# Kernel optimization log

Hardware: AMD Instinct MI355X
Metric: run time of the kernel (lower is better)

The kernel has to match this reference:

```python
import jax, jax.numpy as jnp
import numpy as np


def setup_inputs() -> dict:
    key = jax.random.key(0)
    ks = jax.random.split(key, 8)
    B, L, E = 4096, 200, 64
    H1, H2 = 80, 40
    q = jax.random.normal(ks[0], (B, 1, E), dtype=jnp.float32)
    k = jax.random.normal(ks[1], (B, L, E), dtype=jnp.float32)
    v = jax.random.normal(ks[2], (B, L, E), dtype=jnp.float32)
    mask = jax.random.randint(ks[3], (B, L, 1), 0, 2).astype(bool)
    # Linear weights stored as [in, out] (torch stores [out, in]; math identical)
    W1 = jax.random.normal(ks[4], (4 * E, H1), dtype=jnp.float32) * 0.05
    b1 = jnp.zeros((H1,), dtype=jnp.float32)
    W2 = jax.random.normal(ks[5], (H1, H2), dtype=jnp.float32) * 0.05
    b2 = jnp.zeros((H2,), dtype=jnp.float32)
    Wf = jax.random.normal(ks[6], (H2, 1), dtype=jnp.float32) * 0.05
    bf = jnp.zeros((1,), dtype=jnp.float32)
    return {"q": q, "k": k, "v": v, "mask": mask,
            "W1": W1, "b1": b1, "W2": W2, "b2": b2, "Wf": Wf, "bf": bf}


def reference(q, k, v, mask, W1, b1, W2, b2, Wf, bf):
    # q: [B,1,E] broadcast to [B,L,E]
    qr = jnp.broadcast_to(q, k.shape)
    info = jnp.concatenate([qr, k, qr - k, qr * k], axis=-1)  # [B,L,4E]
    info = info @ W1 + b1                                      # [B,L,H1]
    info = info @ W2 + b2                                      # [B,L,H2]
    info = jax.nn.sigmoid(info)  # single sigmoid after the dense stack, as in source
    logits = info @ Wf + bf                                    # [B,L,1]
    logits = jnp.where(mask, -jnp.inf, logits)
    score = jax.nn.softmax(logits, axis=1)                     # softmax over history dim
    # score^T @ v -> [B,1,E] -> squeeze
    out = jnp.einsum('bl,ble->be', score[..., 0], v)
    return out
```

## Files before the change

kernel.cpp:

```cpp
#include <hip/hip_runtime.h>
#include <hip/hip_bf16.h>
#include <math.h>

namespace {

constexpr int L   = 200;
constexpr int E   = 64;
constexpr int H1N = 80;
constexpr int H2N = 40;

using short8 = __attribute__((ext_vector_type(8))) short;
using f32x4  = __attribute__((ext_vector_type(4))) float;

__device__ inline unsigned short f2bu(float f) {
    return (unsigned short)__builtin_bit_cast(short, __float2bfloat16(f));
}

#define ROR_ADD(x, CTRL) do {                                                   \
    int _t = __builtin_amdgcn_update_dpp(0, __builtin_bit_cast(int, (x)),       \
                                         (CTRL), 0xf, 0xf, true);               \
    (x) += __builtin_bit_cast(float, _t); } while (0)

constexpr int WS_AF   = 0;
constexpr int WS_CF   = 20480;
constexpr int WS_W2F  = 40960;
constexpr int WS_FLAG = 50176;
constexpr int WS_CQ   = 50432;

__global__ void k0_prep(const float* __restrict__ W1,
                        const float* __restrict__ W2,
                        const float* __restrict__ q,
                        const float* __restrict__ b1,
                        const void* __restrict__ mask,
                        float* __restrict__ Af,
                        float* __restrict__ Cf,
                        unsigned short* __restrict__ W2f,
                        float* __restrict__ cq_all,
                        int* __restrict__ flagG, int B)
{
    const int id = blockIdx.x * 256 + threadIdx.x;
    if (id < 640) {
        const int u  = id, cc = u >> 6, ln = u & 63;
        const int nt = cc >> 1, ks = cc & 1;
        const int j  = nt * 16 + (ln & 15);
        const int i0 = ks * 32 + (ln >> 4) * 8;
        #pragma unroll
        for (int e = 0; e < 8; ++e) {
            const int i = i0 + e;
            Af[u * 8 + e] = W1[(E + i) * H1N + j] - W1[(2 * E + i) * H1N + j];
            Cf[u * 8 + e] = W1[(3 * E + i) * H1N + j];
        }
    } else if (id < 1216) {
        const int u   = id - 640, cc = u >> 6, ln = u & 63;
        const int nt2 = cc / 3, ks2 = cc % 3;
        const int n   = nt2 * 16 + (ln & 15);
        const int j0  = ks2 * 32 + (ln >> 4) * 8;
        #pragma unroll
        for (int e = 0; e < 8; ++e) {
            const int j = j0 + e;
            W2f[u * 8 + e] = (j < H1N && n < H2N) ? f2bu(W2[j * H2N + n])
                                                  : (unsigned short)0;
        }
    } else {
        const int t = id - 1216;
        if (t > B * 20) return;
        if (t == B * 20) {
            const unsigned char* mb = (const unsigned char*)mask;
            int isI32 = 1;
            for (int i = 0; i < 256; ++i)
                if ((i & 3) && mb[i]) { isI32 = 0; break; }
            flagG[0] = isI32;
            return;
        }
        const int b  = t / 20;
        const int jq = (t - b * 20) * 4;
        const float* qb = q + (size_t)b * E;
        float4 a = *(const float4*)(b1 + jq);
        #pragma unroll 8
        for (int i = 0; i < E; ++i) {
            const float qv = qb[i];
            const float4 wa = *(const float4*)(W1 + i * H1N + jq);
            const float4 wb = *(const float4*)(W1 + (2 * E + i) * H1N + jq);
            a.x += qv * (wa.x + wb.x);
            a.y += qv * (wa.y + wb.y);
            a.z += qv * (wa.z + wb.z);
            a.w += qv * (wa.w + wb.w);
        }
        *(float4*)(cq_all + (size_t)b * H1N + jq) = a;
    }
}

__global__ __launch_bounds__(512, 6)
void attn_main(const float* __restrict__ q,
               const float* __restrict__ kmat,
               const float* __restrict__ vmat,
               const void* __restrict__ mask,
               const float* __restrict__ b2,
               const float* __restrict__ Wf,
               const float* __restrict__ bfp,
               const float* __restrict__ Af,
               const float* __restrict__ Cf,
               const unsigned short* __restrict__ W2fG,
               const float* __restrict__ cq_all,
               const int* __restrict__ flagG,
               float* __restrict__ out)
{
    const int tid  = threadIdx.x;
    const int lane = tid & 63;
    const int wv   = tid >> 6;
    const int g    = lane >> 4;
    const int c    = lane & 15;

    __shared__ short8 Mt[640];
    __shared__ unsigned short H1t[8][16][104];
    __shared__ float sc[8][16];
    __shared__ float comb_p[8][64];
    __shared__ float comb_s[8];

    const int bb = blockIdx.x;

    *(unsigned long long*)&H1t[wv][c][80 + g * 4] = 0ULL;

    const float* qbase = q + (size_t)bb * E;
    for (int u = tid; u < 640; u += 512) {
        const int cc = u >> 6, ln = u & 63;
        const int i0 = (cc & 1) * 32 + (ln >> 4) * 8;
        const float4 a0 = *(const float4*)(Af + u * 8);
        const float4 a1 = *(const float4*)(Af + u * 8 + 4);
        const float4 c0 = *(const float4*)(Cf + u * 8);
        const float4 c1 = *(const float4*)(Cf + u * 8 + 4);
        const float4 q0 = *(const float4*)(qbase + i0);
        const float4 q1 = *(const float4*)(qbase + i0 + 4);
        short8 h;
        h[0] = (short)f2bu(a0.x + q0.x * c0.x);
        h[1] = (short)f2bu(a0.y + q0.y * c0.y);
        h[2] = (short)f2bu(a0.z + q0.z * c0.z);
        h[3] = (short)f2bu(a0.w + q0.w * c0.w);
        h[4] = (short)f2bu(a1.x + q1.x * c1.x);
        h[5] = (short)f2bu(a1.y + q1.y * c1.y);
        h[6] = (short)f2bu(a1.z + q1.z * c1.z);
        h[7] = (short)f2bu(a1.w + q1.w * c1.w);
        Mt[u] = h;
    }

    const int flagv = flagG[0];
    float cqr[5];
    #pragma unroll
    for (int nt = 0; nt < 5; ++nt)
        cqr[nt] = cq_all[(size_t)bb * H1N + nt * 16 + c];
    float b2r[3], wfr[3];
    #pragma unroll
    for (int nt2 = 0; nt2 < 3; ++nt2) {
        const int nc = nt2 * 16 + c;
        b2r[nt2] = (nc < H2N) ? b2[nc] : 0.f;
        wfr[nt2] = (nc < H2N) ? Wf[nc] : 0.f;
    }
    const float bf0 = bfp[0];
    const short8* W2v = (const short8*)W2fG;
    const float*  kbase = kmat + (size_t)bb * (L * E);
    const float*  vb    = vmat + (size_t)bb * (L * E);
    __syncthreads();

    float s_w = 0.f;
    f32x4 oa = f32x4{0.f, 0.f, 0.f, 0.f};

    #pragma unroll
    for (int rt = 0; rt < 2; ++rt) {
        const int t = wv + 8 * rt;
        if (t < 13) {
            const int row0 = 16 * t;
            const float4* kp = (const float4*)(kbase + (size_t)min(row0 + c, L - 1) * E);
            const float4 kb0 = kp[2 * g];
            const float4 kb1 = kp[2 * g + 1];
            const float4 kb2 = kp[8 + 2 * g];
            const float4 kb3 = kp[8 + 2 * g + 1];

            short8 ak0, ak1;
            ak0[0] = (short)f2bu(kb0.x); ak0[1] = (short)f2bu(kb0.y);
            ak0[2] = (short)f2bu(kb0.z); ak0[3] = (short)f2bu(kb0.w);
            ak0[4] = (short)f2bu(kb1.x); ak0[5] = (short)f2bu(kb1.y);
            ak0[6] = (short)f2bu(kb1.z); ak0[7] = (short)f2bu(kb1.w);
            ak1[0] = (short)f2bu(kb2.x); ak1[1] = (short)f2bu(kb2.y);
            ak1[2] = (short)f2bu(kb2.z); ak1[3] = (short)f2bu(kb2.w);
            ak1[4] = (short)f2bu(kb3.x); ak1[5] = (short)f2bu(kb3.y);
            ak1[6] = (short)f2bu(kb3.z); ak1[7] = (short)f2bu(kb3.w);

            f32x4 acc1[5];
            #pragma unroll
            for (int nt = 0; nt < 5; ++nt) acc1[nt] = f32x4{0.f, 0.f, 0.f, 0.f};
            #pragma unroll
            for (int nt = 0; nt < 5; ++nt) {
                acc1[nt] = __builtin_amdgcn_mfma_f32_16x16x32_bf16(ak0, Mt[(nt * 2 + 0) * 64 + lane], acc1[nt], 0, 0, 0);
                acc1[nt] = __builtin_amdgcn_mfma_f32_16x16x32_bf16(ak1, Mt[(nt * 2 + 1) * 64 + lane], acc1[nt], 0, 0, 0);
            }

            #pragma unroll
            for (int nt = 0; nt < 5; ++nt)
                #pragma unroll
                for (int r = 0; r < 4; ++r)
                    H1t[wv][4 * g + r][nt * 16 + c] = f2bu(acc1[nt][r] + cqr[nt]);

            const float4 v0 = *(const float4*)(vb + (size_t)min(row0 + 0 + g, L - 1) * E + c * 4);
            const float4 v1 = *(const float4*)(vb + (size_t)min(row0 + 4 + g, L - 1) * E + c * 4);
            const float4 v2 = *(const float4*)(vb + (size_t)min(row0 + 8 + g, L - 1) * E + c * 4);
            const float4 v3 = *(const float4*)(vb + (size_t)min(row0 + 12 + g, L - 1) * E + c * 4);

            f32x4 acc2[3];
            #pragma unroll
            for (int nt2 = 0; nt2 < 3; ++nt2) acc2[nt2] = f32x4{0.f, 0.f, 0.f, 0.f};
            #pragma unroll
            for (int ks2 = 0; ks2 < 3; ++ks2) {
                const short8 a2 = *(const short8*)&H1t[wv][c][ks2 * 32 + g * 8];
                #pragma unroll
                for (int nt2 = 0; nt2 < 3; ++nt2)
                    acc2[nt2] = __builtin_amdgcn_mfma_f32_16x16x32_bf16(a2, W2v[(nt2 * 3 + ks2) * 64 + lane], acc2[nt2], 0, 0, 0);
            }

            float pl0 = 0.f, pl1 = 0.f, pl2 = 0.f, pl3 = 0.f;
            #pragma unroll
            for (int nt2 = 0; nt2 < 3; ++nt2) {
                const float wfv = wfr[nt2], b2v = b2r[nt2];
                pl0 += wfv * __builtin_amdgcn_rcpf(1.f + __expf(-(acc2[nt2][0] + b2v)));
                pl1 += wfv * __builtin_amdgcn_rcpf(1.f + __expf(-(acc2[nt2][1] + b2v)));
                pl2 += wfv * __builtin_amdgcn_rcpf(1.f + __expf(-(acc2[nt2][2] + b2v)));
                pl3 += wfv * __builtin_amdgcn_rcpf(1.f + __expf(-(acc2[nt2][3] + b2v)));
            }
            ROR_ADD(pl0, 0x128); ROR_ADD(pl0, 0x124); ROR_ADD(pl0, 0x122); ROR_ADD(pl0, 0x121);
            ROR_ADD(pl1, 0x128); ROR_ADD(pl1, 0x124); ROR_ADD(pl1, 0x122); ROR_ADD(pl1, 0x121);
            ROR_ADD(pl2, 0x128); ROR_ADD(pl2, 0x124); ROR_ADD(pl2, 0x122); ROR_ADD(pl2, 0x121);
            ROR_ADD(pl3, 0x128); ROR_ADD(pl3, 0x124); ROR_ADD(pl3, 0x122); ROR_ADD(pl3, 0x121);

            float p = 0.f;
            const int rowi = row0 + 4 * g + c;
            if (c < 4) {
                if (rowi < L) {
                    const float myv = (c == 0) ? pl0 : (c == 1) ? pl1 : (c == 2) ? pl2 : pl3;
                    const size_t mi = (size_t)bb * L + rowi;
                    const int mv = flagv ? ((const int*)mask)[mi]
                                         : (int)((const unsigned char*)mask)[mi];
                    if (!mv) p = __expf(bf0 + myv);
                }
                sc[wv][4 * g + c] = p;
            }
            float ps = p;
            #pragma unroll
            for (int off = 1; off < 64; off <<= 1)
                ps += __shfl_xor(ps, off);
            s_w += ps;

            const float p0 = sc[wv][0 + g];
            const float p1 = sc[wv][4 + g];
            const float p2 = sc[wv][8 + g];
            const float p3 = sc[wv][12 + g];
            oa[0] += p0 * v0.x + p1 * v1.x + p2 * v2.x + p3 * v3.x;
            oa[1] += p0 * v0.y + p1 * v1.y + p2 * v2.y + p3 * v3.y;
            oa[2] += p0 * v0.z + p1 * v1.z + p2 * v2.z + p3 * v3.z;
            oa[3] += p0 * v0.w + p1 * v1.w + p2 * v2.w + p3 * v3.w;
        }
    }

    #pragma unroll
    for (int j = 0; j < 4; ++j) {
        oa[j] += __shfl_xor(oa[j], 16);
        oa[j] += __shfl_xor(oa[j], 32);
    }
    if (lane < 16)
        *(float4*)&comb_p[wv][4 * lane] = make_float4(oa[0], oa[1], oa[2], oa[3]);
    if (lane == 0) comb_s[wv] = s_w;
    __syncthreads();

    if (tid < 64) {
        float den = comb_s[0];
        float num = comb_p[0][tid];
        #pragma unroll
        for (int w = 1; w < 8; ++w) {
            den += comb_s[w];
            num += comb_p[w][tid];
        }
        out[(size_t)bb * E + tid] = num / den;
    }
}

}

extern "C" void kernel_launch(void* const* d_in, const int* in_sizes, int n_in,
                              void* d_out, int out_size, void* d_ws, size_t ws_size,
                              hipStream_t stream) {
    const float* q  = (const float*)d_in[0];
    const float* k  = (const float*)d_in[1];
    const float* v  = (const float*)d_in[2];
    const void*  mk = d_in[3];
    const float* W1 = (const float*)d_in[4];
    const float* b1 = (const float*)d_in[5];
    const float* W2 = (const float*)d_in[6];
    const float* b2 = (const float*)d_in[7];
    const float* Wf = (const float*)d_in[8];
    const float* bf = (const float*)d_in[9];
    float* out = (float*)d_out;

    const int B = in_sizes[0] / E;

    char* ws = (char*)d_ws;
    float*          Af     = (float*)(ws + WS_AF);
    float*          Cf     = (float*)(ws + WS_CF);
    unsigned short* W2f    = (unsigned short*)(ws + WS_W2F);
    int*            flagG  = (int*)(ws + WS_FLAG);
    float*          cq_all = (float*)(ws + WS_CQ);

    const int prep_ids = 1216 + B * 20 + 1;
    k0_prep<<<(prep_ids + 255) / 256, 256, 0, stream>>>(W1, W2, q, b1, mk,
                                                        Af, Cf, W2f, cq_all, flagG, B);
    attn_main<<<B, 512, 0, stream>>>(q, k, v, mk, b2, Wf, bf,
                                     Af, Cf, W2f, cq_all, flagG, out);
}
```

Measured before the change: 125.1 us.

## Software-pipeline K/V tile loads across the two row tiles per wave

Hoists the first tile's K and V global loads above the setup barrier and issues the second tile's K/V loads before the first tile's MFMA compute, so memory latency overlaps with math. The launch-bounds occupancy hint drops from 6 to 4 to make room for the extra live registers holding the prefetched tiles. This trades occupancy-based latency hiding for explicit prefetch within each wave. The second tile's loads are issued even for waves with no second tile (clamped rows), which adds some redundant traffic.

```diff
diff --git a/kernel.cpp b/kernel.cpp
--- a/kernel.cpp
+++ b/kernel.cpp
@@ -90,7 +90,7 @@
     }
 }
 
-__global__ __launch_bounds__(512, 6)
+__global__ __launch_bounds__(512, 4)
 void attn_main(const float* __restrict__ q,
                const float* __restrict__ kmat,
                const float* __restrict__ vmat,
@@ -159,104 +159,196 @@
     const short8* W2v = (const short8*)W2fG;
     const float*  kbase = kmat + (size_t)bb * (L * E);
     const float*  vb    = vmat + (size_t)bb * (L * E);
+
+    const int tA = wv;
+    const int rowA = 16 * tA;
+    const float4* kpa = (const float4*)(kbase + (size_t)min(rowA + c, L - 1) * E);
+    const float4 ka0 = kpa[2 * g];
+    const float4 ka1 = kpa[2 * g + 1];
+    const float4 ka2 = kpa[8 + 2 * g];
+    const float4 ka3 = kpa[8 + 2 * g + 1];
+    const float4 va0 = *(const float4*)(vb + (size_t)min(rowA + 0 + g, L - 1) * E + c * 4);
+    const float4 va1 = *(const float4*)(vb + (size_t)min(rowA + 4 + g, L - 1) * E + c * 4);
+    const float4 va2 = *(const float4*)(vb + (size_t)min(rowA + 8 + g, L - 1) * E + c * 4);
+    const float4 va3 = *(const float4*)(vb + (size_t)min(rowA + 12 + g, L - 1) * E + c * 4);
     __syncthreads();
 
     float s_w = 0.f;
     f32x4 oa = f32x4{0.f, 0.f, 0.f, 0.f};
 
-    #pragma unroll
-    for (int rt = 0; rt < 2; ++rt) {
-        const int t = wv + 8 * rt;
-        if (t < 13) {
-            const int row0 = 16 * t;
-            const float4* kp = (const float4*)(kbase + (size_t)min(row0 + c, L - 1) * E);
-            const float4 kb0 = kp[2 * g];
-            const float4 kb1 = kp[2 * g + 1];
-            const float4 kb2 = kp[8 + 2 * g];
-            const float4 kb3 = kp[8 + 2 * g + 1];
-
-            short8 ak0, ak1;
-            ak0[0] = (short)f2bu(kb0.x); ak0[1] = (short)f2bu(kb0.y);
-            ak0[2] = (short)f2bu(kb0.z); ak0[3] = (short)f2bu(kb0.w);
-            ak0[4] = (short)f2bu(kb1.x); ak0[5] = (short)f2bu(kb1.y);
-            ak0[6] = (short)f2bu(kb1.z); ak0[7] = (short)f2bu(kb1.w);
-            ak1[0] = (short)f2bu(kb2.x); ak1[1] = (short)f2bu(kb2.y);
-            ak1[2] = (short)f2bu(kb2.z); ak1[3] = (short)f2bu(kb2.w);
-            ak1[4] = (short)f2bu(kb3.x); ak1[5] = (short)f2bu(kb3.y);
-            ak1[6] = (short)f2bu(kb3.z); ak1[7] = (short)f2bu(kb3.w);
-
-            f32x4 acc1[5];
+    float4 kb0, kb1, kb2, kb3, vb0, vb1, vb2, vb3;
+    {
+        const int row0 = rowA;
+        short8 ak0, ak1;
+        ak0[0] = (short)f2bu(ka0.x); ak0[1] = (short)f2bu(ka0.y);
+        ak0[2] = (short)f2bu(ka0.z); ak0[3] = (short)f2bu(ka0.w);
+        ak0[4] = (short)f2bu(ka1.x); ak0[5] = (short)f2bu(ka1.y);
+        ak0[6] = (short)f2bu(ka1.z); ak0[7] = (short)f2bu(ka1.w);
+        ak1[0] = (short)f2bu(ka2.x); ak1[1] = (short)f2bu(ka2.y);
+        ak1[2] = (short)f2bu(ka2.z); ak1[3] = (short)f2bu(ka2.w);
+        ak1[4] = (short)f2bu(ka3.x); ak1[5] = (short)f2bu(ka3.y);
+        ak1[6] = (short)f2bu(ka3.z); ak1[7] = (short)f2bu(ka3.w);
+
+        {
+            const int tB = wv + 8;
+            const int rowB = 16 * tB;
+            const float4* kpb = (const float4*)(kbase + (size_t)min(rowB + c, L - 1) * E);
+            kb0 = kpb[2 * g];
+            kb1 = kpb[2 * g + 1];
+            kb2 = kpb[8 + 2 * g];
+            kb3 = kpb[8 + 2 * g + 1];
+            vb0 = *(const float4*)(vb + (size_t)min(rowB + 0 + g, L - 1) * E + c * 4);
+            vb1 = *(const float4*)(vb + (size_t)min(rowB + 4 + g, L - 1) * E + c * 4);
+            vb2 = *(const float4*)(vb + (size_t)min(rowB + 8 + g, L - 1) * E + c * 4);
+            vb3 = *(const float4*)(vb + (size_t)min(rowB + 12 + g, L - 1) * E + c * 4);
+        }
+
+        f32x4 acc1[5];
+        #pragma unroll
+        for (int nt = 0; nt < 5; ++nt) acc1[nt] = f32x4{0.f, 0.f, 0.f, 0.f};
+        #pragma unroll
+        for (int nt = 0; nt < 5; ++nt) {
+            acc1[nt] = __builtin_amdgcn_mfma_f32_16x16x32_bf16(ak0, Mt[(nt * 2 + 0) * 64 + lane], acc1[nt], 0, 0, 0);
+            acc1[nt] = __builtin_amdgcn_mfma_f32_16x16x32_bf16(ak1, Mt[(nt * 2 + 1) * 64 + lane], acc1[nt], 0, 0, 0);
+        }
+
+        #pragma unroll
+        for (int nt = 0; nt < 5; ++nt)
             #pragma unroll
-            for (int nt = 0; nt < 5; ++nt) acc1[nt] = f32x4{0.f, 0.f, 0.f, 0.f};
+            for (int r = 0; r < 4; ++r)
+                H1t[wv][4 * g + r][nt * 16 + c] = f2bu(acc1[nt][r] + cqr[nt]);
+
+        f32x4 acc2[3];
+        #pragma unroll
+        for (int nt2 = 0; nt2 < 3; ++nt2) acc2[nt2] = f32x4{0.f, 0.f, 0.f, 0.f};
+        #pragma unroll
+        for (int ks2 = 0; ks2 < 3; ++ks2) {
+            const short8 a2 = *(const short8*)&H1t[wv][c][ks2 * 32 + g * 8];
             #pragma unroll
-            for (int nt = 0; nt < 5; ++nt) {
-                acc1[nt] = __builtin_amdgcn_mfma_f32_16x16x32_bf16(ak0, Mt[(nt * 2 + 0) * 64 + lane], acc1[nt], 0, 0, 0);
-                acc1[nt] = __builtin_amdgcn_mfma_f32_16x16x32_bf16(ak1, Mt[(nt * 2 + 1) * 64 + lane], acc1[nt], 0, 0, 0);
+            for (int nt2 = 0; nt2 < 3; ++nt2)
+                acc2[nt2] = __builtin_amdgcn_mfma_f32_16x16x32_bf16(a2, W2v[(nt2 * 3 + ks2) * 64 + lane], acc2[nt2], 0, 0, 0);
+        }
+
+        float pl0 = 0.f, pl1 = 0.f, pl2 = 0.f, pl3 = 0.f;
+        #pragma unroll
+        for (int nt2 = 0; nt2 < 3; ++nt2) {
+            const float wfv = wfr[nt2], b2v = b2r[nt2];
+            pl0 += wfv * __builtin_amdgcn_rcpf(1.f + __expf(-(acc2[nt2][0] + b2v)));
+            pl1 += wfv * __builtin_amdgcn_rcpf(1.f + __expf(-(acc2[nt2][1] + b2v)));
+            pl2 += wfv * __builtin_amdgcn_rcpf(1.f + __expf(-(acc2[nt2][2] + b2v)));
+            pl3 += wfv * __builtin_amdgcn_rcpf(1.f + __expf(-(acc2[nt2][3] + b2v)));
+        }
+        ROR_ADD(pl0, 0x128); ROR_ADD(pl0, 0x124); ROR_ADD(pl0, 0x122); ROR_ADD(pl0, 0x121);
+        ROR_ADD(pl1, 0x128); ROR_ADD(pl1, 0x124); ROR_ADD(pl1, 0x122); ROR_ADD(pl1, 0x121);
+        ROR_ADD(pl2, 0x128); ROR_ADD(pl2, 0x124); ROR_ADD(pl2, 0x122); ROR_ADD(pl2, 0x121);
+        ROR_ADD(pl3, 0x128); ROR_ADD(pl3, 0x124); ROR_ADD(pl3, 0x122); ROR_ADD(pl3, 0x121);
+
+        float p = 0.f;
+        const int rowi = row0 + 4 * g + c;
+        if (c < 4) {
+            if (rowi < L) {
+                const float myv = (c == 0) ? pl0 : (c == 1) ? pl1 : (c == 2) ? pl2 : pl3;
+                const size_t mi = (size_t)bb * L + rowi;
+                const int mv = flagv ? ((const int*)mask)[mi]
+                                     : (int)((const unsigned char*)mask)[mi];
+                if (!mv) p = __expf(bf0 + myv);
             }
-
+            sc[wv][4 * g + c] = p;
+        }
+        float ps = p;
+        #pragma unroll
+        for (int off = 1; off < 64; off <<= 1)
+            ps += __shfl_xor(ps, off);
+        s_w += ps;
+
+        const float p0 = sc[wv][0 + g];
+        const float p1 = sc[wv][4 + g];
+        const float p2 = sc[wv][8 + g];
+        const float p3 = sc[wv][12 + g];
+        oa[0] += p0 * va0.x + p1 * va1.x + p2 * va2.x + p3 * va3.x;
+        oa[1] += p0 * va0.y + p1 * va1.y + p2 * va2.y + p3 * va3.y;
+        oa[2] += p0 * va0.z + p1 * va1.z + p2 * va2.z + p3 * va3.z;
+        oa[3] += p0 * va0.w + p1 * va1.w + p2 * va2.w + p3 * va3.w;
+    }
+
+    if (wv + 8 < 13) {
+        const int row0 = 16 * (wv + 8);
+        short8 ak0, ak1;
+        ak0[0] = (short)f2bu(kb0.x); ak0[1] = (short)f2bu(kb0.y);
+        ak0[2] = (short)f2bu(kb0.z); ak0[3] = (short)f2bu(kb0.w);
+        ak0[4] = (short)f2bu(kb1.x); ak0[5] = (short)f2bu(kb1.y);
+        ak0[6] = (short)f2bu(kb1.z); ak0[7] = (short)f2bu(kb1.w);
+        ak1[0] = (short)f2bu(kb2.x); ak1[1] = (short)f2bu(kb2.y);
+        ak1[2] = (short)f2bu(kb2.z); ak1[3] = (short)f2bu(kb2.w);
+        ak1[4] = (short)f2bu(kb3.x); ak1[5] = (short)f2bu(kb3.y);
+        ak1[6] = (short)f2bu(kb3.z); ak1[7] = (short)f2bu(kb3.w);
+
+        f32x4 acc1[5];
+        #pragma unroll
+        for (int nt = 0; nt < 5; ++nt) acc1[nt] = f32x4{0.f, 0.f, 0.f, 0.f};
+        #pragma unroll
+        for (int nt = 0; nt < 5; ++nt) {
+            acc1[nt] = __builtin_amdgcn_mfma_f32_16x16x32_bf16(ak0, Mt[(nt * 2 + 0) * 64 + lane], acc1[nt], 0, 0, 0);
+            acc1[nt] = __builtin_amdgcn_mfma_f32_16x16x32_bf16(ak1, Mt[(nt * 2 + 1) * 64 + lane], acc1[nt], 0, 0, 0);
+        }
+
+        #pragma unroll
+        for (int nt = 0; nt < 5; ++nt)
             #pragma unroll
-            for (int nt = 0; nt < 5; ++nt)
-                #pragma unroll
-                for (int r = 0; r < 4; ++r)
-                    H1t[wv][4 * g + r][nt * 16 + c] = f2bu(acc1[nt][r] + cqr[nt]);
-
-            const float4 v0 = *(const float4*)(vb + (size_t)min(row0 + 0 + g, L - 1) * E + c * 4);
-            const float4 v1 = *(const float4*)(vb + (size_t)min(row0 + 4 + g, L - 1) * E + c * 4);
-            const float4 v2 = *(const float4*)(vb + (size_t)min(row0 + 8 + g, L - 1) * E + c * 4);
-            const float4 v3 = *(const float4*)(vb + (size_t)min(row0 + 12 + g, L - 1) * E + c * 4);
-
-            f32x4 acc2[3];
+            for (int r = 0; r < 4; ++r)
+                H1t[wv][4 * g + r][nt * 16 + c] = f2bu(acc1[nt][r] + cqr[nt]);
+
+        f32x4 acc2[3];
+        #pragma unroll
+        for (int nt2 = 0; nt2 < 3; ++nt2) acc2[nt2] = f32x4{0.f, 0.f, 0.f, 0.f};
+        #pragma unroll
+        for (int ks2 = 0; ks2 < 3; ++ks2) {
+            const short8 a2 = *(const short8*)&H1t[wv][c][ks2 * 32 + g * 8];
             #pragma unroll
-            for (int nt2 = 0; nt2 < 3; ++nt2) acc2[nt2] = f32x4{0.f, 0.f, 0.f, 0.f};
-            #pragma unroll
-            for (int ks2 = 0; ks2 < 3; ++ks2) {
-                const short8 a2 = *(const short8*)&H1t[wv][c][ks2 * 32 + g * 8];
-                #pragma unroll
-                for (int nt2 = 0; nt2 < 3; ++nt2)
-                    acc2[nt2] = __builtin_amdgcn_mfma_f32_16x16x32_bf16(a2, W2v[(nt2 * 3 + ks2) * 64 + lane], acc2[nt2], 0, 0, 0);
+            for (int nt2 = 0; nt2 < 3; ++nt2)
+                acc2[nt2] = __builtin_amdgcn_mfma_f32_16x16x32_bf16(a2, W2v[(nt2 * 3 + ks2) * 64 + lane], acc2[nt2], 0, 0, 0);
+        }
+
+        float pl0 = 0.f, pl1 = 0.f, pl2 = 0.f, pl3 = 0.f;
+        #pragma unroll
+        for (int nt2 = 0; nt2 < 3; ++nt2) {
+            const float wfv = wfr[nt2], b2v = b2r[nt2];
+            pl0 += wfv * __builtin_amdgcn_rcpf(1.f + __expf(-(acc2[nt2][0] + b2v)));
+            pl1 += wfv * __builtin_amdgcn_rcpf(1.f + __expf(-(acc2[nt2][1] + b2v)));
+            pl2 += wfv * __builtin_amdgcn_rcpf(1.f + __expf(-(acc2[nt2][2] + b2v)));
+            pl3 += wfv * __builtin_amdgcn_rcpf(1.f + __expf(-(acc2[nt2][3] + b2v)));
+        }
+        ROR_ADD(pl0, 0x128); ROR_ADD(pl0, 0x124); ROR_ADD(pl0, 0x122); ROR_ADD(pl0, 0x121);
+        ROR_ADD(pl1, 0x128); ROR_ADD(pl1, 0x124); ROR_ADD(pl1, 0x122); ROR_ADD(pl1, 0x121);
+        ROR_ADD(pl2, 0x128); ROR_ADD(pl2, 0x124); ROR_ADD(pl2, 0x122); ROR_ADD(pl2, 0x121);
+        ROR_ADD(pl3, 0x128); ROR_ADD(pl3, 0x124); ROR_ADD(pl3, 0x122); ROR_ADD(pl3, 0x121);
+
+        float p = 0.f;
+        const int rowi = row0 + 4 * g + c;
+        if (c < 4) {
+            if (rowi < L) {
+                const float myv = (c == 0) ? pl0 : (c == 1) ? pl1 : (c == 2) ? pl2 : pl3;
+                const size_t mi = (size_t)bb * L + rowi;
+                const int mv = flagv ? ((const int*)mask)[mi]
+                                     : (int)((const unsigned char*)mask)[mi];
+                if (!mv) p = __expf(bf0 + myv);
             }
-
-            float pl0 = 0.f, pl1 = 0.f, pl2 = 0.f, pl3 = 0.f;
-            #pragma unroll
-            for (int nt2 = 0; nt2 < 3; ++nt2) {
-                const float wfv = wfr[nt2], b2v = b2r[nt2];
-                pl0 += wfv * __builtin_amdgcn_rcpf(1.f + __expf(-(acc2[nt2][0] + b2v)));
-                pl1 += wfv * __builtin_amdgcn_rcpf(1.f + __expf(-(acc2[nt2][1] + b2v)));
-                pl2 += wfv * __builtin_amdgcn_rcpf(1.f + __expf(-(acc2[nt2][2] + b2v)));
-                pl3 += wfv * __builtin_amdgcn_rcpf(1.f + __expf(-(acc2[nt2][3] + b2v)));
-            }
-            ROR_ADD(pl0, 0x128); ROR_ADD(pl0, 0x124); ROR_ADD(pl0, 0x122); ROR_ADD(pl0, 0x121);
-            ROR_ADD(pl1, 0x128); ROR_ADD(pl1, 0x124); ROR_ADD(pl1, 0x122); ROR_ADD(pl1, 0x121);
-            ROR_ADD(pl2, 0x128); ROR_ADD(pl2, 0x124); ROR_ADD(pl2, 0x122); ROR_ADD(pl2, 0x121);
-            ROR_ADD(pl3, 0x128); ROR_ADD(pl3, 0x124); ROR_ADD(pl3, 0x122); ROR_ADD(pl3, 0x121);
-
-            float p = 0.f;
-            const int rowi = row0 + 4 * g + c;
-            if (c < 4) {
-                if (rowi < L) {
-                    const float myv = (c == 0) ? pl0 : (c == 1) ? pl1 : (c == 2) ? pl2 : pl3;
-                    const size_t mi = (size_t)bb * L + rowi;
-                    const int mv = flagv ? ((const int*)mask)[mi]
-                                         : (int)((const unsigned char*)mask)[mi];
-                    if (!mv) p = __expf(bf0 + myv);
-                }
-                sc[wv][4 * g + c] = p;
-            }
-            float ps = p;
-            #pragma unroll
-            for (int off = 1; off < 64; off <<= 1)
-                ps += __shfl_xor(ps, off);
-            s_w += ps;
-
-            const float p0 = sc[wv][0 + g];
-            const float p1 = sc[wv][4 + g];
-            const float p2 = sc[wv][8 + g];
-            const float p3 = sc[wv][12 + g];
-            oa[0] += p0 * v0.x + p1 * v1.x + p2 * v2.x + p3 * v3.x;
-            oa[1] += p0 * v0.y + p1 * v1.y + p2 * v2.y + p3 * v3.y;
-            oa[2] += p0 * v0.z + p1 * v1.z + p2 * v2.z + p3 * v3.z;
-            oa[3] += p0 * v0.w + p1 * v1.w + p2 * v2.w + p3 * v3.w;
-        }
+            sc[wv][4 * g + c] = p;
+        }
+        float ps = p;
+        #pragma unroll
+        for (int off = 1; off < 64; off <<= 1)
+            ps += __shfl_xor(ps, off);
+        s_w += ps;
+
+        const float p0 = sc[wv][0 + g];
+        const float p1 = sc[wv][4 + g];
+        const float p2 = sc[wv][8 + g];
+        const float p3 = sc[wv][12 + g];
+        oa[0] += p0 * vb0.x + p1 * vb1.x + p2 * vb2.x + p3 * vb3.x;
+        oa[1] += p0 * vb0.y + p1 * vb1.y + p2 * vb2.y + p3 * vb3.y;
+        oa[2] += p0 * vb0.z + p1 * vb1.z + p2 * vb2.z + p3 * vb3.z;
+        oa[3] += p0 * vb0.w + p1 * vb1.w + p2 * vb2.w + p3 * vb3.w;
     }
 
     #pragma unroll
```

After: 123.5 us. No clear change (-1.3%).
